# Optimization experiments

Measured on AMD Instinct MI355X. Metric: run time of the kernel, lower is better.

The kernel has to match this reference:

```python
import jax, jax.numpy as jnp
import numpy as np

N, F_NODE, F_EDGE = 1024, 64, 32
F_IN = 2 * F_NODE + F_EDGE  # 160


def setup_inputs() -> dict:
    key = jax.random.key(0)
    ks = jax.random.split(key, 6)
    H = jax.random.normal(ks[0], (N, F_NODE), dtype=jnp.float32)
    A = jax.random.randint(ks[1], (N, N), 0, 2).astype(jnp.float32)
    E = jax.random.normal(ks[2], (N, N, F_EDGE), dtype=jnp.float32)
    # params: reset_parameters_uniform -> U(-s, s), s = 1/sqrt(dim0)
    s = 1.0 / np.sqrt(F_IN)
    W = jax.random.uniform(ks[3], (F_IN, F_NODE), jnp.float32, -s, s)
    W_att = jax.random.uniform(ks[4], (F_IN, F_NODE), jnp.float32, -s, s)
    sb = 1.0 / np.sqrt(F_NODE)
    bias = jax.random.uniform(ks[5], (F_NODE,), jnp.float32, -sb, sb)
    return {"H": H, "A": A, "E": E, "W": W, "W_att": W_att, "bias": bias}


def reference(H, A, E, W, W_att, bias):
    n = H.shape[0]
    # all-pairs concat: HE[a,b] = [H[a], H[b], E[a,b]]  -> [N, N, 2F+Fe]
    H_row = jnp.broadcast_to(H[:, None, :], (n, n, H.shape[1]))  # H2: repeat over dim 1
    H_col = jnp.broadcast_to(H[None, :, :], (n, n, H.shape[1]))  # H1: repeat over dim 0
    HE = jnp.concatenate([H_row, H_col, E], axis=2) * A[:, :, None]
    Hp = jnp.einsum('abi,ij->abj', HE, W) + bias
    Ha = jnp.einsum('abi,ij->abj', HE, W_att) + bias
    gated = jax.nn.relu(Hp) * jax.nn.sigmoid(Ha)
    return jnp.sum(gated, axis=1)
```

## Files before the change

kernel.cpp:

```cpp
#include <hip/hip_runtime.h>

#define NN 1024
#define FN 64
#define FE 32

typedef __bf16 bf16x8 __attribute__((ext_vector_type(8)));
typedef short  short8 __attribute__((ext_vector_type(8)));
typedef float  f32x4  __attribute__((ext_vector_type(4)));

static __device__ __forceinline__ unsigned short f2b(float x){
    unsigned int u = __float_as_uint(x);
    unsigned int r = (u + 0x7fffu + ((u >> 16) & 1u)) >> 16;
    return (unsigned short)r;
}

static __device__ __forceinline__ float fast_sigmoid(float y){
    return __builtin_amdgcn_rcpf(1.0f + __expf(-y));
}

__global__ void prep_nodes(const float* __restrict__ H, const float* __restrict__ W,
                           const float* __restrict__ Wa, const float* __restrict__ bias,
                           float* __restrict__ P1b, float* __restrict__ P2,
                           float* __restrict__ Q1b, float* __restrict__ Q2){
    int a = blockIdx.x, j = threadIdx.x;
    __shared__ float h[FN];
    h[j] = H[a*FN + j];
    __syncthreads();
    float s1 = 0.f, s2 = 0.f, s3 = 0.f, s4 = 0.f;
    #pragma unroll
    for (int k = 0; k < FN; k++){
        float hk = h[k];
        s1 = fmaf(hk, W [k*FN + j],        s1);
        s2 = fmaf(hk, W [(FN + k)*FN + j], s2);
        s3 = fmaf(hk, Wa[k*FN + j],        s3);
        s4 = fmaf(hk, Wa[(FN + k)*FN + j], s4);
    }
    float bj = bias[j];
    P1b[a*FN + j] = s1 + bj;
    P2 [a*FN + j] = s2;
    Q1b[a*FN + j] = s3 + bj;
    Q2 [a*FN + j] = s4;
}

__global__ void prep_wedge(const float* __restrict__ W, const float* __restrict__ Wa,
                           unsigned short* __restrict__ WtE, unsigned short* __restrict__ WtA){
    int j = threadIdx.x;
    const float* src = blockIdx.x ? Wa : W;
    unsigned short* dst = blockIdx.x ? WtA : WtE;
    #pragma unroll
    for (int k = 0; k < FE; k++)
        dst[j*FE + k] = f2b(src[(2*FN + k)*FN + j]);
}

__global__ __launch_bounds__(256) void mga_main(
    const float* __restrict__ A, const float* __restrict__ E,
    const float* __restrict__ P1b, const float* __restrict__ P2,
    const float* __restrict__ Q1b, const float* __restrict__ Q2,
    const unsigned short* __restrict__ WtE, const unsigned short* __restrict__ WtA,
    const float* __restrict__ bias, float* __restrict__ out)
{
    int a    = blockIdx.x;
    int tid  = threadIdx.x;
    int wave = tid >> 6, lane = tid & 63;
    int col  = lane & 15, quad = lane >> 4;

    __shared__ float arow[NN];
    __shared__ float red[16*FN];

    ((float4*)arow)[tid] = ((const float4*)(A + (size_t)a*NN))[tid];

    float c1[4], d1[4], g0[4], acc[4];
    #pragma unroll
    for (int t = 0; t < 4; t++){
        int j = t*16 + col;
        c1[t] = P1b[a*FN + j];
        d1[t] = Q1b[a*FN + j];
        float bj = bias[j];
        g0[t] = fmaxf(bj, 0.f) * fast_sigmoid(bj);
        acc[t] = 0.f;
    }

    bf16x8 bw[4], ba[4];
    #pragma unroll
    for (int t = 0; t < 4; t++){
        int n = t*16 + col;
        bw[t] = __builtin_bit_cast(bf16x8, *(const short8*)(WtE + n*FE + quad*8));
        ba[t] = __builtin_bit_cast(bf16x8, *(const short8*)(WtA + n*FE + quad*8));
    }

    __syncthreads();

    const f32x4 zero = {0.f, 0.f, 0.f, 0.f};

    for (int c = 0; c < 16; c++){
        int b0 = c*64;

        const float* ep = E + ((size_t)a*NN + (b0 + wave*16 + col))*FE + quad*8;
        float4 e0 = *(const float4*)(ep);
        float4 e1 = *(const float4*)(ep + 4);
        short8 afs;
        afs[0] = (short)f2b(e0.x); afs[1] = (short)f2b(e0.y);
        afs[2] = (short)f2b(e0.z); afs[3] = (short)f2b(e0.w);
        afs[4] = (short)f2b(e1.x); afs[5] = (short)f2b(e1.y);
        afs[6] = (short)f2b(e1.z); afs[7] = (short)f2b(e1.w);
        bf16x8 af = __builtin_bit_cast(bf16x8, afs);

        f32x4 pw[4], pa[4];
        #pragma unroll
        for (int t = 0; t < 4; t++){
            pw[t] = __builtin_amdgcn_mfma_f32_16x16x32_bf16(af, bw[t], zero, 0, 0, 0);
            pa[t] = __builtin_amdgcn_mfma_f32_16x16x32_bf16(af, ba[t], zero, 0, 0, 0);
        }

        int bbase = b0 + wave*16 + quad*4;
        float av[4];
        #pragma unroll
        for (int r = 0; r < 4; r++) av[r] = arow[bbase + r];

        #pragma unroll
        for (int t = 0; t < 4; t++){
            int j = t*16 + col;
            #pragma unroll
            for (int r = 0; r < 4; r++){
                float sx = pw[t][r] + c1[t] + P2[(bbase + r)*FN + j];
                float sy = pa[t][r] + d1[t] + Q2[(bbase + r)*FN + j];
                float f  = fmaxf(sx, 0.f) * fast_sigmoid(sy);
                acc[t] += (av[r] != 0.f) ? f : g0[t];
            }
        }
    }

    #pragma unroll
    for (int t = 0; t < 4; t++)
        red[(wave*4 + quad)*FN + t*16 + col] = acc[t];
    __syncthreads();
    if (tid < FN){
        float s = 0.f;
        #pragma unroll
        for (int r = 0; r < 16; r++) s += red[r*FN + tid];
        out[a*FN + tid] = s;
    }
}

extern "C" void kernel_launch(void* const* d_in, const int* in_sizes, int n_in,
                              void* d_out, int out_size, void* d_ws, size_t ws_size,
                              hipStream_t stream) {
    const float* H    = (const float*)d_in[0];
    const float* A    = (const float*)d_in[1];
    const float* E    = (const float*)d_in[2];
    const float* W    = (const float*)d_in[3];
    const float* Wa   = (const float*)d_in[4];
    const float* bias = (const float*)d_in[5];
    float* out = (float*)d_out;

    float* ws  = (float*)d_ws;
    float* P1b = ws;
    float* P2  = ws + 1*NN*FN;
    float* Q1b = ws + 2*NN*FN;
    float* Q2  = ws + 3*NN*FN;
    unsigned short* WtE = (unsigned short*)(ws + 4*NN*FN);
    unsigned short* WtA = WtE + FN*FE;

    prep_nodes<<<dim3(NN), dim3(FN), 0, stream>>>(H, W, Wa, bias, P1b, P2, Q1b, Q2);
    prep_wedge<<<dim3(2),  dim3(FN), 0, stream>>>(W, Wa, WtE, WtA);
    mga_main  <<<dim3(NN), dim3(256), 0, stream>>>(A, E, P1b, P2, Q1b, Q2, WtE, WtA, bias, out);
}
```

Measured before the change: 280.4 us.

## Compute node projections on MFMA inside main kernel instead of precomputed fp32 tables

The fp32 node-projection tables P2/Q2, which were gathered per edge row, are removed. The H[b] contribution is now computed per tile with extra bf16 MFMAs over K=64, and the H[a] plus bias term is computed once per block with MFMA. Each wave now covers 32 rows and 32 output columns instead of 16 rows and 64 columns, and the two prep kernels are merged into one that converts H and transposes the weights to bf16. This trades global memory traffic for extra matrix-core work, and it lowers precision by rounding H and the node weights to bf16.

```diff
diff --git a/kernel.cpp b/kernel.cpp
--- a/kernel.cpp
+++ b/kernel.cpp
@@ -3,6 +3,7 @@
 #define NN 1024
 #define FN 64
 #define FE 32
+#define FIN 160
 
 typedef __bf16 bf16x8 __attribute__((ext_vector_type(8)));
 typedef short  short8 __attribute__((ext_vector_type(8)));
@@ -18,44 +19,35 @@
     return __builtin_amdgcn_rcpf(1.0f + __expf(-y));
 }
 
-__global__ void prep_nodes(const float* __restrict__ H, const float* __restrict__ W,
-                           const float* __restrict__ Wa, const float* __restrict__ bias,
-                           float* __restrict__ P1b, float* __restrict__ P2,
-                           float* __restrict__ Q1b, float* __restrict__ Q2){
-    int a = blockIdx.x, j = threadIdx.x;
-    __shared__ float h[FN];
-    h[j] = H[a*FN + j];
-    __syncthreads();
-    float s1 = 0.f, s2 = 0.f, s3 = 0.f, s4 = 0.f;
-    #pragma unroll
-    for (int k = 0; k < FN; k++){
-        float hk = h[k];
-        s1 = fmaf(hk, W [k*FN + j],        s1);
-        s2 = fmaf(hk, W [(FN + k)*FN + j], s2);
-        s3 = fmaf(hk, Wa[k*FN + j],        s3);
-        s4 = fmaf(hk, Wa[(FN + k)*FN + j], s4);
-    }
-    float bj = bias[j];
-    P1b[a*FN + j] = s1 + bj;
-    P2 [a*FN + j] = s2;
-    Q1b[a*FN + j] = s3 + bj;
-    Q2 [a*FN + j] = s4;
+static __device__ __forceinline__ bf16x8 ldfrag(const unsigned short* p){
+    return __builtin_bit_cast(bf16x8, *(const short8*)p);
 }
 
-__global__ void prep_wedge(const float* __restrict__ W, const float* __restrict__ Wa,
-                           unsigned short* __restrict__ WtE, unsigned short* __restrict__ WtA){
-    int j = threadIdx.x;
-    const float* src = blockIdx.x ? Wa : W;
-    unsigned short* dst = blockIdx.x ? WtA : WtE;
-    #pragma unroll
-    for (int k = 0; k < FE; k++)
-        dst[j*FE + k] = f2b(src[(2*FN + k)*FN + j]);
+__global__ void prep(const float* __restrict__ H, const float* __restrict__ W,
+                     const float* __restrict__ Wa,
+                     unsigned short* __restrict__ Hb,
+                     unsigned short* __restrict__ WtE,
+                     unsigned short* __restrict__ WtA){
+    int bid = blockIdx.x, tid = threadIdx.x;
+    if (bid < 64){
+        int i = (bid*256 + tid)*4;
+        float4 v = *(const float4*)(H + i);
+        ushort4 o;
+        o.x = f2b(v.x); o.y = f2b(v.y); o.z = f2b(v.z); o.w = f2b(v.w);
+        *(ushort4*)(Hb + i) = o;
+    } else {
+        const float* src = (bid == 64) ? W : Wa;
+        unsigned short* dst = (bid == 64) ? WtE : WtA;
+        for (int idx = tid; idx < FIN*FN; idx += 256){
+            int k = idx >> 6, j = idx & 63;
+            dst[j*FIN + k] = f2b(src[idx]);
+        }
+    }
 }
 
 __global__ __launch_bounds__(256) void mga_main(
     const float* __restrict__ A, const float* __restrict__ E,
-    const float* __restrict__ P1b, const float* __restrict__ P2,
-    const float* __restrict__ Q1b, const float* __restrict__ Q2,
+    const unsigned short* __restrict__ Hb,
     const unsigned short* __restrict__ WtE, const unsigned short* __restrict__ WtA,
     const float* __restrict__ bias, float* __restrict__ out)
 {
@@ -63,81 +55,100 @@
     int tid  = threadIdx.x;
     int wave = tid >> 6, lane = tid & 63;
     int col  = lane & 15, quad = lane >> 4;
+    int half = wave >> 1, mh = wave & 1;
 
     __shared__ float arow[NN];
     __shared__ float red[16*FN];
 
     ((float4*)arow)[tid] = ((const float4*)(A + (size_t)a*NN))[tid];
 
-    float c1[4], d1[4], g0[4], acc[4];
+    bf16x8 Bw[2][3], Ba[2][3];
     #pragma unroll
-    for (int t = 0; t < 4; t++){
-        int j = t*16 + col;
-        c1[t] = P1b[a*FN + j];
-        d1[t] = Q1b[a*FN + j];
-        float bj = bias[j];
-        g0[t] = fmaxf(bj, 0.f) * fast_sigmoid(bj);
-        acc[t] = 0.f;
+    for (int tl = 0; tl < 2; tl++){
+        int n = (2*half + tl)*16 + col;
+        #pragma unroll
+        for (int s = 0; s < 3; s++){
+            Bw[tl][s] = ldfrag(WtE + n*FIN + (s+2)*32 + quad*8);
+            Ba[tl][s] = ldfrag(WtA + n*FIN + (s+2)*32 + quad*8);
+        }
     }
 
-    bf16x8 bw[4], ba[4];
+    bf16x8 ha0 = ldfrag(Hb + a*FN + quad*8);
+    bf16x8 ha1 = ldfrag(Hb + a*FN + 32 + quad*8);
+    const f32x4 zero = {0.f, 0.f, 0.f, 0.f};
+    f32x4 cw[2], ca[2];
+    float g0[2], acc[2];
     #pragma unroll
-    for (int t = 0; t < 4; t++){
-        int n = t*16 + col;
-        bw[t] = __builtin_bit_cast(bf16x8, *(const short8*)(WtE + n*FE + quad*8));
-        ba[t] = __builtin_bit_cast(bf16x8, *(const short8*)(WtA + n*FE + quad*8));
+    for (int tl = 0; tl < 2; tl++){
+        int n = (2*half + tl)*16 + col;
+        float bj = bias[n];
+        f32x4 cb = {bj, bj, bj, bj};
+        bf16x8 b0 = ldfrag(WtE + n*FIN + quad*8);
+        bf16x8 b1 = ldfrag(WtE + n*FIN + 32 + quad*8);
+        cw[tl] = __builtin_amdgcn_mfma_f32_16x16x32_bf16(ha1, b1,
+                 __builtin_amdgcn_mfma_f32_16x16x32_bf16(ha0, b0, cb, 0,0,0), 0,0,0);
+        b0 = ldfrag(WtA + n*FIN + quad*8);
+        b1 = ldfrag(WtA + n*FIN + 32 + quad*8);
+        ca[tl] = __builtin_amdgcn_mfma_f32_16x16x32_bf16(ha1, b1,
+                 __builtin_amdgcn_mfma_f32_16x16x32_bf16(ha0, b0, cb, 0,0,0), 0,0,0);
+        g0[tl] = fmaxf(bj, 0.f) * fast_sigmoid(bj);
+        acc[tl] = 0.f;
     }
 
     __syncthreads();
 
-    const f32x4 zero = {0.f, 0.f, 0.f, 0.f};
+    for (int c = 0; c < 16; c++){
+        int b0r = c*64;
 
-    for (int c = 0; c < 16; c++){
-        int b0 = c*64;
-
-        const float* ep = E + ((size_t)a*NN + (b0 + wave*16 + col))*FE + quad*8;
-        float4 e0 = *(const float4*)(ep);
-        float4 e1 = *(const float4*)(ep + 4);
-        short8 afs;
-        afs[0] = (short)f2b(e0.x); afs[1] = (short)f2b(e0.y);
-        afs[2] = (short)f2b(e0.z); afs[3] = (short)f2b(e0.w);
-        afs[4] = (short)f2b(e1.x); afs[5] = (short)f2b(e1.y);
-        afs[6] = (short)f2b(e1.z); afs[7] = (short)f2b(e1.w);
-        bf16x8 af = __builtin_bit_cast(bf16x8, afs);
-
-        f32x4 pw[4], pa[4];
+        bf16x8 ef[2], hb0[2], hb1[2];
         #pragma unroll
-        for (int t = 0; t < 4; t++){
-            pw[t] = __builtin_amdgcn_mfma_f32_16x16x32_bf16(af, bw[t], zero, 0, 0, 0);
-            pa[t] = __builtin_amdgcn_mfma_f32_16x16x32_bf16(af, ba[t], zero, 0, 0, 0);
+        for (int mt = 0; mt < 2; mt++){
+            int brow = b0r + mh*32 + mt*16 + col;
+            const float* ep = E + ((size_t)a*NN + brow)*FE + quad*8;
+            float4 e0 = *(const float4*)(ep);
+            float4 e1 = *(const float4*)(ep + 4);
+            short8 afs;
+            afs[0]=(short)f2b(e0.x); afs[1]=(short)f2b(e0.y);
+            afs[2]=(short)f2b(e0.z); afs[3]=(short)f2b(e0.w);
+            afs[4]=(short)f2b(e1.x); afs[5]=(short)f2b(e1.y);
+            afs[6]=(short)f2b(e1.z); afs[7]=(short)f2b(e1.w);
+            ef[mt]  = __builtin_bit_cast(bf16x8, afs);
+            hb0[mt] = ldfrag(Hb + brow*FN + quad*8);
+            hb1[mt] = ldfrag(Hb + brow*FN + 32 + quad*8);
         }
 
-        int bbase = b0 + wave*16 + quad*4;
-        float av[4];
         #pragma unroll
-        for (int r = 0; r < 4; r++) av[r] = arow[bbase + r];
-
-        #pragma unroll
-        for (int t = 0; t < 4; t++){
-            int j = t*16 + col;
+        for (int mt = 0; mt < 2; mt++){
+            float4 av = *(const float4*)(arow + b0r + mh*32 + mt*16 + quad*4);
             #pragma unroll
-            for (int r = 0; r < 4; r++){
-                float sx = pw[t][r] + c1[t] + P2[(bbase + r)*FN + j];
-                float sy = pa[t][r] + d1[t] + Q2[(bbase + r)*FN + j];
-                float f  = fmaxf(sx, 0.f) * fast_sigmoid(sy);
-                acc[t] += (av[r] != 0.f) ? f : g0[t];
+            for (int tl = 0; tl < 2; tl++){
+                f32x4 pw = __builtin_amdgcn_mfma_f32_16x16x32_bf16(ef[mt], Bw[tl][2],
+                           __builtin_amdgcn_mfma_f32_16x16x32_bf16(hb1[mt], Bw[tl][1],
+                           __builtin_amdgcn_mfma_f32_16x16x32_bf16(hb0[mt], Bw[tl][0],
+                               cw[tl], 0,0,0), 0,0,0), 0,0,0);
+                f32x4 pa = __builtin_amdgcn_mfma_f32_16x16x32_bf16(ef[mt], Ba[tl][2],
+                           __builtin_amdgcn_mfma_f32_16x16x32_bf16(hb1[mt], Ba[tl][1],
+                           __builtin_amdgcn_mfma_f32_16x16x32_bf16(hb0[mt], Ba[tl][0],
+                               ca[tl], 0,0,0), 0,0,0), 0,0,0);
+                float* avp = (float*)&av;
+                #pragma unroll
+                for (int r = 0; r < 4; r++){
+                    float f = fmaxf(pw[r], 0.f) * fast_sigmoid(pa[r]);
+                    acc[tl] += (avp[r] != 0.f) ? f : g0[tl];
+                }
             }
         }
     }
 
     #pragma unroll
-    for (int t = 0; t < 4; t++)
-        red[(wave*4 + quad)*FN + t*16 + col] = acc[t];
+    for (int tl = 0; tl < 2; tl++)
+        red[(wave*4 + quad)*FN + (2*half + tl)*16 + col] = acc[tl];
     __syncthreads();
     if (tid < FN){
+        int base = (tid >= 32) ? 8 : 0;
         float s = 0.f;
         #pragma unroll
-        for (int r = 0; r < 16; r++) s += red[r*FN + tid];
+        for (int r = 0; r < 8; r++) s += red[(base + r)*FN + tid];
         out[a*FN + tid] = s;
     }
 }
@@ -153,15 +164,10 @@
     const float* bias = (const float*)d_in[5];
     float* out = (float*)d_out;
 
-    float* ws  = (float*)d_ws;
-    float* P1b = ws;
-    float* P2  = ws + 1*NN*FN;
-    float* Q1b = ws + 2*NN*FN;
-    float* Q2  = ws + 3*NN*FN;
-    unsigned short* WtE = (unsigned short*)(ws + 4*NN*FN);
-    unsigned short* WtA = WtE + FN*FE;
+    unsigned short* Hb  = (unsigned short*)d_ws;
+    unsigned short* WtE = Hb + NN*FN;
+    unsigned short* WtA = WtE + FN*FIN;
 
-    prep_nodes<<<dim3(NN), dim3(FN), 0, stream>>>(H, W, Wa, bias, P1b, P2, Q1b, Q2);
-    prep_wedge<<<dim3(2),  dim3(FN), 0, stream>>>(W, Wa, WtE, WtA);
-    mga_main  <<<dim3(NN), dim3(256), 0, stream>>>(A, E, P1b, P2, Q1b, Q2, WtE, WtA, bias, out);
+    prep    <<<dim3(66),   dim3(256), 0, stream>>>(H, W, Wa, Hb, WtE, WtA);
+    mga_main<<<dim3(NN),   dim3(256), 0, stream>>>(A, E, Hb, WtE, WtA, bias, out);
 }
```

New measurement: 270.2 us. -3.6%, faster.
